# Kernel tuning notes

Measured on AMD Instinct MI355X. Metric: run time of the kernel, lower is better.

The kernel has to match this reference:

```python
import jax, jax.numpy as jnp
import numpy as np

BN_EPS = 1e-5

def batchnorm2d(x, gamma, beta):
    # x: [B, H, *, *]; normalize over (B, dim2, dim3) per channel H (training-mode batch stats)
    mean = jnp.mean(x, axis=(0, 2, 3), keepdims=True)
    var = jnp.var(x, axis=(0, 2, 3), keepdims=True)
    xhat = (x - mean) * jax.lax.rsqrt(var + BN_EPS)
    return xhat * gamma[None, :, None, None] + beta[None, :, None, None]

def setup_inputs() -> dict:
    key = jax.random.key(0)
    ks = jax.random.split(key, 8)
    B, N, C = 64, 196, 768
    H = 12
    hd = C // H  # 64
    patch = 196  # img_size**2, must equal N
    x = jax.random.normal(ks[0], (B, N, C), dtype=jnp.float32)
    W_qv = jax.random.normal(ks[1], (C, 2 * C), dtype=jnp.float32) * (1.0 / np.sqrt(C))
    k_ext = jax.random.normal(ks[2], (patch, hd), dtype=jnp.float32)  # torch init: ones; randomized for testing
    attn_bias = jax.random.normal(ks[3], (1, patch), dtype=jnp.float32) * 0.02
    bn_gamma = jnp.ones((H,), dtype=jnp.float32) + 0.1 * jax.random.normal(ks[4], (H,), dtype=jnp.float32)
    bn_beta = 0.1 * jax.random.normal(ks[5], (H,), dtype=jnp.float32)
    W_proj = jax.random.normal(ks[6], (C, C), dtype=jnp.float32) * (1.0 / np.sqrt(C))
    b_proj = jnp.zeros((C,), dtype=jnp.float32)
    return {"x": x, "W_qv": W_qv, "k_ext": k_ext, "attn_bias": attn_bias,
            "bn_gamma": bn_gamma, "bn_beta": bn_beta, "W_proj": W_proj, "b_proj": b_proj}

def reference(x, W_qv, k_ext, attn_bias, bn_gamma, bn_beta, W_proj, b_proj):
    B, N, C = x.shape
    H = bn_gamma.shape[0]
    hd = C // H
    scale = hd ** -0.5
    # qv projection: [B,N,2C] -> q,v each [B,H,N,hd]
    qv = (x @ W_qv).reshape(B, N, 2, H, hd).transpose(2, 0, 3, 1, 4)
    q, v = qv[0], qv[1]
    # scores against fixed k_ext: [B,H,N,patch]
    attn = jnp.einsum('bhnd,pd->bhnp', q, k_ext)
    attn = (batchnorm2d(attn, bn_gamma, bn_beta) + attn_bias) * scale
    attn = jax.nn.softmax(attn, axis=-1)
    v = batchnorm2d(v, bn_gamma, bn_beta)
    out = jnp.einsum('bhnp,bhpd->bhnd', attn, v)  # patch == N
    out = out.transpose(0, 2, 1, 3).reshape(B, N, C)
    return out @ W_proj + b_proj
```

## Files before the change

### kernel.cpp

```cpp
#include <hip/hip_runtime.h>
#include <hip/hip_bf16.h>

typedef __bf16 b16;
typedef __bf16 b16x4 __attribute__((ext_vector_type(4)));
typedef __bf16 b16x8 __attribute__((ext_vector_type(8)));
typedef float  f32x4 __attribute__((ext_vector_type(4)));

#define B_   64
#define N_   196
#define C_   768
#define H_   12
#define HD_  64
#define TOK  (B_*N_)
#define SCALE 0.125f

__device__ __forceinline__ void gl_lds16(const void* g, void* l){
  __builtin_amdgcn_global_load_lds((const __attribute__((address_space(1))) void*)g,
                                   (__attribute__((address_space(3))) void*)l, 16, 0, 0);
}

__global__ __launch_bounds__(256) void k_transpose_cvt(const float* __restrict__ in,
                                                       b16* __restrict__ out, int R, int C){
  __shared__ b16 tile[32][33];
  int tx = threadIdx.x, ty = threadIdx.y;
  int bx = blockIdx.x, by = blockIdx.y;
  int c = bx*32 + tx;
  #pragma unroll
  for (int i = 0; i < 32; i += 8){
    int r = by*32 + ty + i;
    tile[ty+i][tx] = (b16)in[(long)r*C + c];
  }
  __syncthreads();
  int rr = by*32 + tx;
  #pragma unroll
  for (int i = 0; i < 32; i += 8){
    int cc = bx*32 + ty + i;
    out[(long)cc*R + rr] = tile[tx][ty+i];
  }
}

__global__ __launch_bounds__(256) void k_cvt(const float* __restrict__ in, b16* __restrict__ out){
  long i = ((long)blockIdx.x*256 + threadIdx.x)*8;
  const float4* s = (const float4*)(in + i);
  float4 f0 = s[0], f1 = s[1];
  b16x8 v; v[0]=(b16)f0.x; v[1]=(b16)f0.y; v[2]=(b16)f0.z; v[3]=(b16)f0.w;
           v[4]=(b16)f1.x; v[5]=(b16)f1.y; v[6]=(b16)f1.z; v[7]=(b16)f1.w;
  *(b16x8*)(out + i) = v;
}

__global__ __launch_bounds__(256) void k_kprep(const float* __restrict__ k_ext,
                                               float* __restrict__ Kmat, float* __restrict__ ksum){
  __shared__ float ks[N_][HD_];
  int tid = threadIdx.x, blk = blockIdx.x;
  for (int i = tid; i < N_*HD_; i += 256) ks[i/HD_][i%HD_] = k_ext[i];
  __syncthreads();
  int i = tid >> 2;
  int j0 = blk*16 + (tid & 3)*4;
  float a0=0.f, a1=0.f, a2=0.f, a3=0.f;
  for (int p = 0; p < N_; ++p){
    float ki = ks[p][i];
    float4 kv = *(const float4*)&ks[p][j0];
    a0 += ki*kv.x; a1 += ki*kv.y; a2 += ki*kv.z; a3 += ki*kv.w;
  }
  Kmat[i*64+j0+0]=a0; Kmat[i*64+j0+1]=a1; Kmat[i*64+j0+2]=a2; Kmat[i*64+j0+3]=a3;
  if (blk == 0 && tid < 64){
    float s = 0.f;
    for (int p = 0; p < N_; ++p) s += ks[p][tid];
    ksum[tid] = s;
  }
}

template<int MODE>
__global__ __launch_bounds__(256) void k_gemm(const b16* __restrict__ A,
                                              const b16* __restrict__ BT,
                                              b16* __restrict__ qout, b16* __restrict__ vout,
                                              float* __restrict__ fout, const float* __restrict__ bias,
                                              const float* __restrict__ ksum, float* __restrict__ stats){
  const int NT  = (MODE == 0) ? 12 : 6;
  const int NWG = 98*NT;
  int orig = blockIdx.x;
  int q8 = NWG >> 3, r8 = NWG & 7;
  int xcd = orig & 7, loc = orig >> 3;
  int bid = (xcd < r8 ? xcd*(q8+1) : r8*(q8+1) + (xcd-r8)*q8) + loc;
  int rt = bid / NT, ct = bid % NT;
  int brow = rt*128, bcol = ct*128;

  __shared__ b16 sm[2][2][128*32];
  int tid = threadIdx.x, lane = tid & 63, w = tid >> 6;
  int wr = w >> 1, wc = w & 1;

  int rsub = w*16 + (lane>>2);
  int gsrc = (lane & 3) ^ ((lane >> 3) & 3);
  const b16* gA = A  + (long)(brow + rsub)*768 + gsrc*8;
  const b16* gB = BT + (long)(bcol + rsub)*768 + gsrc*8;
  b16* lA0 = &sm[0][0][w*16*32];
  b16* lB0 = &sm[0][1][w*16*32];
  b16* lA1 = &sm[1][0][w*16*32];
  b16* lB1 = &sm[1][1][w*16*32];

#define STAGE(la, lb, kt) do{ \
    gl_lds16(gA + (kt)*32,            (la));        \
    gl_lds16(gA + (kt)*32 + 64*768,   (la) + 64*32);\
    gl_lds16(gB + (kt)*32,            (lb));        \
    gl_lds16(gB + (kt)*32 + 64*768,   (lb) + 64*32);\
  } while(0)

#define COMPUTE(cur) do{ \
    const char* smA = (const char*)sm[cur][0]; \
    const char* smB = (const char*)sm[cur][1]; \
    b16x8 af[4], bf[4]; \
    _Pragma("unroll") \
    for (int m = 0; m < 4; ++m){ \
      int row = wr*64 + m*16 + (lane & 15); \
      af[m] = *(const b16x8*)(smA + row*64 + (((lane>>4) ^ ((row>>1)&3))<<4)); \
    } \
    _Pragma("unroll") \
    for (int n = 0; n < 4; ++n){ \
      int row = wc*64 + n*16 + (lane & 15); \
      bf[n] = *(const b16x8*)(smB + row*64 + (((lane>>4) ^ ((row>>1)&3))<<4)); \
    } \
    _Pragma("unroll") \
    for (int m = 0; m < 4; ++m) \
      _Pragma("unroll") \
      for (int n = 0; n < 4; ++n) \
        acc[m][n] = __builtin_amdgcn_mfma_f32_16x16x32_bf16(bf[n], af[m], acc[m][n], 0, 0, 0); \
  } while(0)

  f32x4 acc[4][4];
  #pragma unroll
  for (int m = 0; m < 4; ++m)
    #pragma unroll
    for (int n = 0; n < 4; ++n) acc[m][n] = (f32x4){0.f,0.f,0.f,0.f};

  STAGE(lA0, lB0, 0);
  STAGE(lA1, lB1, 1);

  #pragma unroll 1
  for (int kt = 0; kt < 23; ++kt){
    int cur = kt & 1;
    asm volatile("s_waitcnt vmcnt(4)" ::: "memory");
    __builtin_amdgcn_s_barrier();
    asm volatile("" ::: "memory");
    COMPUTE(cur);
    asm volatile("" ::: "memory");
    __builtin_amdgcn_s_barrier();
    asm volatile("" ::: "memory");
    if (kt < 22){
      if (cur == 0) STAGE(lA0, lB0, kt+2);
      else          STAGE(lA1, lB1, kt+2);
    }
  }
  asm volatile("s_waitcnt vmcnt(0)" ::: "memory");
  __builtin_amdgcn_s_barrier();
  asm volatile("" ::: "memory");
  COMPUTE(1);
#undef COMPUTE
#undef STAGE

  if constexpr (MODE == 0){
    bool isV = (bcol >= 768);
    b16* dst = isV ? vout : qout;
    int cb0 = bcol - (isV ? 768 : 0) + wc*64;
    #pragma unroll
    for (int m = 0; m < 4; ++m){
      int r2 = brow + wr*64 + m*16 + (lane & 15);
      #pragma unroll
      for (int n = 0; n < 4; ++n){
        int cc = cb0 + n*16 + ((lane>>4)<<2);
        b16x4 pv;
        #pragma unroll
        for (int j = 0; j < 4; ++j) pv[j] = (b16)acc[m][n][j];
        *(b16x4*)(dst + (long)r2*768 + cc) = pv;
      }
    }
    {
      float a_acc = 0.f, b_acc = 0.f;
      #pragma unroll
      for (int n = 0; n < 4; ++n)
        #pragma unroll
        for (int j = 0; j < 4; ++j){
          int d = n*16 + ((lane>>4)<<2) + j;
          float s = 0.f, s2 = 0.f;
          #pragma unroll
          for (int m = 0; m < 4; ++m){
            float v = acc[m][n][j];
            s += v; s2 += v*v;
          }
          if (isV){ a_acc += s; b_acc += s2; }
          else      a_acc += s * ksum[d];
        }
      #pragma unroll
      for (int off = 1; off < 64; off <<= 1){
        a_acc += __shfl_xor(a_acc, off, 64);
        b_acc += __shfl_xor(b_acc, off, 64);
      }
      if (lane == 0){
        if (isV){
          int hv = 2*(ct - 6) + wc;
          atomicAdd(&stats[24 + hv], a_acc);
          atomicAdd(&stats[36 + hv], b_acc);
        } else {
          int hq = 2*ct + wc;
          atomicAdd(&stats[hq], a_acc);
        }
      }
    }
  } else {
    #pragma unroll
    for (int m = 0; m < 4; ++m){
      int r2 = brow + wr*64 + m*16 + (lane & 15);
      #pragma unroll
      for (int n = 0; n < 4; ++n){
        int cc = bcol + wc*64 + n*16 + ((lane>>4)<<2);
        f32x4 bv = *(const f32x4*)(bias + cc);
        f32x4 o;
        #pragma unroll
        for (int j = 0; j < 4; ++j) o[j] = acc[m][n][j] + bv[j];
        *(f32x4*)(fout + (long)r2*768 + cc) = o;
      }
    }
  }
}

__global__ __launch_bounds__(256) void k_gram(const b16* __restrict__ qb, float* __restrict__ G){
  __shared__ b16 qT[64*232];
  int tid = threadIdx.x, lane = tid & 63, w = tid >> 6;
  int h = blockIdx.x % 12, bg = blockIdx.x / 12;
  f32x4 acc[4];
  #pragma unroll
  for (int n = 0; n < 4; ++n) acc[n] = (f32x4){0.f,0.f,0.f,0.f};
  #pragma unroll 1
  for (int r = 0; r < 2; ++r){
    int b = bg*2 + r;
    const b16* src = qb + (long)(b*196)*768 + h*64;
    int d = lane;
    for (int p0 = w*8; p0 < 224; p0 += 32){
      b16x8 w8;
      #pragma unroll
      for (int j = 0; j < 8; ++j){
        int p = p0 + j;
        w8[j] = (p < 196) ? src[(long)p*768 + d] : (b16)0.f;
      }
      *(b16x8*)(qT + d*232 + p0) = w8;
    }
    __syncthreads();
    #pragma unroll
    for (int ks = 0; ks < 7; ++ks){
      int t0 = ks*32;
      b16x8 af = *(const b16x8*)(qT + (16*w + (lane&15))*232 + t0 + ((lane>>4)<<3));
      #pragma unroll
      for (int n = 0; n < 4; ++n){
        b16x8 bf = *(const b16x8*)(qT + (16*n + (lane&15))*232 + t0 + ((lane>>4)<<3));
        acc[n] = __builtin_amdgcn_mfma_f32_16x16x32_bf16(af, bf, acc[n], 0, 0, 0);
      }
    }
    __syncthreads();
  }
  float* Gh = G + h*4096;
  #pragma unroll
  for (int n = 0; n < 4; ++n)
    #pragma unroll
    for (int j = 0; j < 4; ++j){
      int i  = 16*w + ((lane>>4)<<2) + j;
      int jj = 16*n + (lane&15);
      atomicAdd(&Gh[i*64 + jj], acc[n][j]);
    }
}

__global__ __launch_bounds__(256) void k_sfin(const float* __restrict__ G, const float* __restrict__ Kmat,
                                              const float* __restrict__ stats, const float* __restrict__ gamma,
                                              const float* __restrict__ beta, float* __restrict__ coef){
  int h = blockIdx.x, tid = threadIdx.x;
  const float* Gh = G + h*4096;
  float s = 0.f;
  #pragma unroll
  for (int k = 0; k < 16; ++k) s += Gh[tid + k*256]*Kmat[tid + k*256];
  #pragma unroll
  for (int off = 1; off < 64; off <<= 1) s += __shfl_xor(s, off, 64);
  __shared__ float red[4];
  if ((tid & 63) == 0) red[tid>>6] = s;
  __syncthreads();
  if (tid == 0){
    float S2 = red[0]+red[1]+red[2]+red[3];
    const float cntS = 2458624.f, cntV = 802816.f;
    float S1 = stats[h], VS = stats[24+h], VS2 = stats[36+h];
    float ms = S1/cntS;
    float vars = S2/cntS - ms*ms;
    float alpha = gamma[h]*SCALE*rsqrtf(vars + 1e-5f);
    float mv = VS/cntV;
    float varv = VS2/cntV - mv*mv;
    float a = gamma[h]*rsqrtf(varv + 1e-5f);
    coef[h*4+0] = alpha;
    coef[h*4+1] = a;
    coef[h*4+2] = beta[h] - a*mv;
  }
}

__global__ __launch_bounds__(256, 2) void k_attn(const b16* __restrict__ qb, const b16* __restrict__ vb,
                                                 const float* __restrict__ k_ext,
                                                 const float* __restrict__ attn_bias,
                                                 const float* __restrict__ coef,
                                                 b16* __restrict__ Ob){
  __shared__ b16 ksh[196*64];
  __shared__ b16 vsh[64*216];
  __shared__ b16 psh[4][16*200];
  __shared__ float bsh[196];

  int tid = threadIdx.x, lane = tid & 63, wid = tid >> 6;
  int bh = blockIdx.x;
  int h = bh % 12, b = bh / 12;
  const b16* qt = qb + (long)(b*196)*768 + h*64;
  const b16* vt = vb + (long)(b*196)*768 + h*64;
  float alpha = coef[h*4+0], av = coef[h*4+1], cv = coef[h*4+2];

  for (int c = tid; c < 196*8; c += 256){
    int p = c >> 3, g = c & 7;
    const float4* src = (const float4*)(k_ext + p*64 + g*8);
    float4 f0 = src[0], f1 = src[1];
    b16x8 v; v[0]=(b16)f0.x; v[1]=(b16)f0.y; v[2]=(b16)f0.z; v[3]=(b16)f0.w;
             v[4]=(b16)f1.x; v[5]=(b16)f1.y; v[6]=(b16)f1.z; v[7]=(b16)f1.w;
    *(b16x8*)((char*)ksh + p*128 + ((g ^ (p&7))<<4)) = v;
  }
  for (int p = tid; p < 196; p += 256) bsh[p] = attn_bias[p]*SCALE;
  {
    int d = tid & 63;
    for (int p0 = (tid>>6)*8; p0 < 196; p0 += 32){
      b16x8 w;
      #pragma unroll
      for (int j = 0; j < 8; ++j){
        int p = p0 + j;
        w[j] = (p < 196) ? vt[(long)p*768 + d] : (b16)0.f;
      }
      *(b16x8*)((char*)vsh + d*432 + p0*2) = w;
    }
  }
  __syncthreads();

  for (int rt = wid; rt < 13; rt += 4){
    int n0 = rt*16;
    int qrow = n0 + (lane & 15); if (qrow > 195) qrow = 195;
    b16x8 a0 = *(const b16x8*)((const char*)qt + (long)qrow*1536 +      ((lane>>4)<<4));
    b16x8 a1 = *(const b16x8*)((const char*)qt + (long)qrow*1536 + 64 + ((lane>>4)<<4));

    f32x4 sc[13];
    #pragma unroll
    for (int ct = 0; ct < 13; ++ct){
      int p = ct*16 + (lane & 15); int pc = p > 195 ? 195 : p;
      b16x8 b0 = *(const b16x8*)((const char*)ksh + pc*128 + ((( (lane>>4))   ^ (pc&7))<<4));
      b16x8 b1 = *(const b16x8*)((const char*)ksh + pc*128 + (((4+(lane>>4))  ^ (pc&7))<<4));
      f32x4 z = {0.f,0.f,0.f,0.f};
      z = __builtin_amdgcn_mfma_f32_16x16x32_bf16(a0, b0, z, 0, 0, 0);
      z = __builtin_amdgcn_mfma_f32_16x16x32_bf16(a1, b1, z, 0, 0, 0);
      sc[ct] = z;
    }
    int pcol = lane & 15;
    float mx[4] = {-1e30f,-1e30f,-1e30f,-1e30f};
    #pragma unroll
    for (int ct = 0; ct < 13; ++ct){
      int p = ct*16 + pcol;
      bool valid = (p < 196);
      float badd = valid ? bsh[p < 196 ? p : 0] : 0.f;
      #pragma unroll
      for (int j = 0; j < 4; ++j){
        float lv = valid ? (sc[ct][j]*alpha + badd) : -1e30f;
        sc[ct][j] = lv;
        mx[j] = fmaxf(mx[j], lv);
      }
    }
    #pragma unroll
    for (int off = 1; off < 16; off <<= 1)
      #pragma unroll
      for (int j = 0; j < 4; ++j) mx[j] = fmaxf(mx[j], __shfl_xor(mx[j], off, 64));
    float sm[4] = {0.f,0.f,0.f,0.f};
    #pragma unroll
    for (int ct = 0; ct < 13; ++ct)
      #pragma unroll
      for (int j = 0; j < 4; ++j){
        float e = __expf(sc[ct][j] - mx[j]);
        sc[ct][j] = e; sm[j] += e;
      }
    #pragma unroll
    for (int off = 1; off < 16; off <<= 1)
      #pragma unroll
      for (int j = 0; j < 4; ++j) sm[j] += __shfl_xor(sm[j], off, 64);
    float rs[4];
    #pragma unroll
    for (int j = 0; j < 4; ++j) rs[j] = 1.f/sm[j];

    b16* pw = psh[wid];
    #pragma unroll
    for (int ct = 0; ct < 12; ++ct){
      int p = ct*16 + pcol;
      #pragma unroll
      for (int j = 0; j < 4; ++j){
        int r = ((lane>>4)<<2) + j;
        pw[r*200 + p] = (b16)(sc[ct][j]*rs[j]);
      }
    }
    float pt12[4];
    #pragma unroll
    for (int j = 0; j < 4; ++j) pt12[j] = sc[12][j]*rs[j];

    __asm__ volatile("s_waitcnt lgkmcnt(0)" ::: "memory");
    __builtin_amdgcn_sched_barrier(0);

    f32x4 o[4];
    #pragma unroll
    for (int dt = 0; dt < 4; ++dt) o[dt] = (f32x4){0.f,0.f,0.f,0.f};
    #pragma unroll
    for (int pt = 0; pt < 6; ++pt){
      b16x8 pa = *(const b16x8*)((const char*)pw + (lane&15)*400 + pt*64 + ((lane>>4)<<4));
      #pragma unroll
      for (int dt = 0; dt < 4; ++dt){
        b16x8 vf = *(const b16x8*)((const char*)vsh + (dt*16 + (lane&15))*432 + pt*64 + ((lane>>4)<<4));
        o[dt] = __builtin_amdgcn_mfma_f32_16x16x32_bf16(pa, vf, o[dt], 0, 0, 0);
      }
    }
    #pragma unroll
    for (int e = 0; e < 4; ++e){
      float pe[4];
      #pragma unroll
      for (int j = 0; j < 4; ++j) pe[j] = __shfl(pt12[j], (lane & 48) + e, 64);
      #pragma unroll
      for (int dt = 0; dt < 4; ++dt){
        b16 vv = *((const b16*)((const char*)vsh + (dt*16 + (lane&15))*432 + (192+e)*2));
        float vvf = (float)vv;
        #pragma unroll
        for (int j = 0; j < 4; ++j) o[dt][j] += pe[j]*vvf;
      }
    }
    #pragma unroll
    for (int dt = 0; dt < 4; ++dt)
      #pragma unroll
      for (int j = 0; j < 4; ++j){
        int n = n0 + ((lane>>4)<<2) + j;
        if (n < 196){
          long idx = ((long)(b*196 + n))*768 + h*64 + dt*16 + (lane&15);
          Ob[idx] = (b16)(av*o[dt][j] + cv);
        }
      }
  }
}

extern "C" void kernel_launch(void* const* d_in, const int* in_sizes, int n_in,
                              void* d_out, int out_size, void* d_ws, size_t ws_size,
                              hipStream_t stream){
  const float* x         = (const float*)d_in[0];
  const float* W_qv      = (const float*)d_in[1];
  const float* k_ext     = (const float*)d_in[2];
  const float* attn_bias = (const float*)d_in[3];
  const float* bn_gamma  = (const float*)d_in[4];
  const float* bn_beta   = (const float*)d_in[5];
  const float* W_proj    = (const float*)d_in[6];
  const float* b_proj    = (const float*)d_in[7];
  float* out = (float*)d_out;

  char* ws = (char*)d_ws;
  const long SZ = 19267584;
  b16*   q_buf   = (b16*)(ws);
  b16*   v_buf   = (b16*)(ws + SZ);
  b16*   O_buf   = (b16*)(ws + 2*SZ);
  b16*   x_bf16  = (b16*)(ws + 2*SZ);
  b16*   W_qvT   = (b16*)(ws + 3*SZ);
  b16*   W_projT = (b16*)(ws + 3*SZ + 2359296);
  float* Kmat    = (float*)(ws + 3*SZ + 3538944);
  float* ksum    = Kmat + 4096;
  float* stats   = ksum + 64;
  float* coef    = stats + 48;
  float* Ggram   = coef + 48;

  hipMemsetAsync(stats, 0, 48*sizeof(float), stream);
  hipMemsetAsync(Ggram, 0, 12*4096*sizeof(float), stream);

  dim3 tb(32, 8);
  k_transpose_cvt<<<dim3(1536/32, 768/32), tb, 0, stream>>>(W_qv,   W_qvT,   768, 1536);
  k_transpose_cvt<<<dim3(768/32,  768/32), tb, 0, stream>>>(W_proj, W_projT, 768, 768);
  k_cvt<<<4704, 256, 0, stream>>>(x, x_bf16);
  k_kprep<<<4, 256, 0, stream>>>(k_ext, Kmat, ksum);
  k_gemm<0><<<98*12, 256, 0, stream>>>(x_bf16, W_qvT, q_buf, v_buf, nullptr, nullptr, ksum, stats);
  k_gram<<<384, 256, 0, stream>>>(q_buf, Ggram);
  k_sfin<<<12, 256, 0, stream>>>(Ggram, Kmat, stats, bn_gamma, bn_beta, coef);
  k_attn<<<768, 256, 0, stream>>>(q_buf, v_buf, k_ext, attn_bias, coef, O_buf);
  k_gemm<1><<<98*6, 256, 0, stream>>>(O_buf, W_projT, nullptr, nullptr, out, b_proj, nullptr, nullptr);
}
```

Measured before the change: 196.6 us.

## Replace LDS double-buffered GEMM staging with direct global-to-register MFMA operand loads

The GEMM kernel drops the shared-memory double buffer fed by global_load_lds, along with its barriers. Each wave now loads its MFMA A and B fragments straight from global memory into registers, with the k-loop unrolled by four. This removes LDS traffic and workgroup synchronisation. In exchange the two waves that share a row or column tile each fetch it separately, and loads lose the coalesced, swizzled staging, so more pressure falls on the L2 cache and global bandwidth.

Result: slower. 288.0 us (+46.5%).

```diff
diff --git a/kernel.cpp b/kernel.cpp
--- a/kernel.cpp
+++ b/kernel.cpp
@@ -13,11 +13,6 @@
 #define HD_  64
 #define TOK  (B_*N_)
 #define SCALE 0.125f
-
-__device__ __forceinline__ void gl_lds16(const void* g, void* l){
-  __builtin_amdgcn_global_load_lds((const __attribute__((address_space(1))) void*)g,
-                                   (__attribute__((address_space(3))) void*)l, 16, 0, 0);
-}
 
 __global__ __launch_bounds__(256) void k_transpose_cvt(const float* __restrict__ in,
                                                        b16* __restrict__ out, int R, int C){
@@ -83,48 +78,14 @@
   int xcd = orig & 7, loc = orig >> 3;
   int bid = (xcd < r8 ? xcd*(q8+1) : r8*(q8+1) + (xcd-r8)*q8) + loc;
   int rt = bid / NT, ct = bid % NT;
-  int brow = rt*128, bcol = ct*128;
-
-  __shared__ b16 sm[2][2][128*32];
+
   int tid = threadIdx.x, lane = tid & 63, w = tid >> 6;
   int wr = w >> 1, wc = w & 1;
-
-  int rsub = w*16 + (lane>>2);
-  int gsrc = (lane & 3) ^ ((lane >> 3) & 3);
-  const b16* gA = A  + (long)(brow + rsub)*768 + gsrc*8;
-  const b16* gB = BT + (long)(bcol + rsub)*768 + gsrc*8;
-  b16* lA0 = &sm[0][0][w*16*32];
-  b16* lB0 = &sm[0][1][w*16*32];
-  b16* lA1 = &sm[1][0][w*16*32];
-  b16* lB1 = &sm[1][1][w*16*32];
-
-#define STAGE(la, lb, kt) do{ \
-    gl_lds16(gA + (kt)*32,            (la));        \
-    gl_lds16(gA + (kt)*32 + 64*768,   (la) + 64*32);\
-    gl_lds16(gB + (kt)*32,            (lb));        \
-    gl_lds16(gB + (kt)*32 + 64*768,   (lb) + 64*32);\
-  } while(0)
-
-#define COMPUTE(cur) do{ \
-    const char* smA = (const char*)sm[cur][0]; \
-    const char* smB = (const char*)sm[cur][1]; \
-    b16x8 af[4], bf[4]; \
-    _Pragma("unroll") \
-    for (int m = 0; m < 4; ++m){ \
-      int row = wr*64 + m*16 + (lane & 15); \
-      af[m] = *(const b16x8*)(smA + row*64 + (((lane>>4) ^ ((row>>1)&3))<<4)); \
-    } \
-    _Pragma("unroll") \
-    for (int n = 0; n < 4; ++n){ \
-      int row = wc*64 + n*16 + (lane & 15); \
-      bf[n] = *(const b16x8*)(smB + row*64 + (((lane>>4) ^ ((row>>1)&3))<<4)); \
-    } \
-    _Pragma("unroll") \
-    for (int m = 0; m < 4; ++m) \
-      _Pragma("unroll") \
-      for (int n = 0; n < 4; ++n) \
-        acc[m][n] = __builtin_amdgcn_mfma_f32_16x16x32_bf16(bf[n], af[m], acc[m][n], 0, 0, 0); \
-  } while(0)
+  int brow = rt*128 + wr*64;
+  int bcol = ct*128 + wc*64;
+
+  const b16* pa = A  + (long)(brow + (lane & 15))*768 + ((lane >> 4) << 3);
+  const b16* pb = BT + (long)(bcol + (lane & 15))*768 + ((lane >> 4) << 3);
 
   f32x4 acc[4][4];
   #pragma unroll
@@ -132,38 +93,27 @@
     #pragma unroll
     for (int n = 0; n < 4; ++n) acc[m][n] = (f32x4){0.f,0.f,0.f,0.f};
 
-  STAGE(lA0, lB0, 0);
-  STAGE(lA1, lB1, 1);
-
-  #pragma unroll 1
-  for (int kt = 0; kt < 23; ++kt){
-    int cur = kt & 1;
-    asm volatile("s_waitcnt vmcnt(4)" ::: "memory");
-    __builtin_amdgcn_s_barrier();
-    asm volatile("" ::: "memory");
-    COMPUTE(cur);
-    asm volatile("" ::: "memory");
-    __builtin_amdgcn_s_barrier();
-    asm volatile("" ::: "memory");
-    if (kt < 22){
-      if (cur == 0) STAGE(lA0, lB0, kt+2);
-      else          STAGE(lA1, lB1, kt+2);
-    }
-  }
-  asm volatile("s_waitcnt vmcnt(0)" ::: "memory");
-  __builtin_amdgcn_s_barrier();
-  asm volatile("" ::: "memory");
-  COMPUTE(1);
-#undef COMPUTE
-#undef STAGE
+  #pragma unroll 4
+  for (int kt = 0; kt < 24; ++kt){
+    b16x8 af[4], bf[4];
+    #pragma unroll
+    for (int m = 0; m < 4; ++m) af[m] = *(const b16x8*)(pa + (long)m*16*768 + kt*32);
+    #pragma unroll
+    for (int n = 0; n < 4; ++n) bf[n] = *(const b16x8*)(pb + (long)n*16*768 + kt*32);
+    #pragma unroll
+    for (int m = 0; m < 4; ++m)
+      #pragma unroll
+      for (int n = 0; n < 4; ++n)
+        acc[m][n] = __builtin_amdgcn_mfma_f32_16x16x32_bf16(bf[n], af[m], acc[m][n], 0, 0, 0);
+  }
 
   if constexpr (MODE == 0){
     bool isV = (bcol >= 768);
     b16* dst = isV ? vout : qout;
-    int cb0 = bcol - (isV ? 768 : 0) + wc*64;
+    int cb0 = bcol - (isV ? 768 : 0);
     #pragma unroll
     for (int m = 0; m < 4; ++m){
-      int r2 = brow + wr*64 + m*16 + (lane & 15);
+      int r2 = brow + m*16 + (lane & 15);
       #pragma unroll
       for (int n = 0; n < 4; ++n){
         int cc = cb0 + n*16 + ((lane>>4)<<2);
@@ -208,10 +158,10 @@
   } else {
     #pragma unroll
     for (int m = 0; m < 4; ++m){
-      int r2 = brow + wr*64 + m*16 + (lane & 15);
+      int r2 = brow + m*16 + (lane & 15);
       #pragma unroll
       for (int n = 0; n < 4; ++n){
-        int cc = bcol + wc*64 + n*16 + ((lane>>4)<<2);
+        int cc = bcol + n*16 + ((lane>>4)<<2);
         f32x4 bv = *(const f32x4*)(bias + cc);
         f32x4 o;
         #pragma unroll
```

## Enlarge GEMM tiles to 256x256 with 512-thread workgroups

Applied to the files above, without the earlier changes.

Both bf16 GEMMs (qv projection and output projection) now use 256x256 output tiles computed by 8 waves in a 2x4 layout, each wave holding an 8x4 grid of 16x16 MFMA accumulators. The goal is better operand reuse from LDS and less global traffic per FLOP. The trade-off is far fewer workgroups (294 and 147) on a 256-CU part, which leaves CUs idle or unevenly loaded. It also raises register pressure through 128 accumulator floats per lane and adds an lgkmcnt wait before the barrier.

Measured after the change: 194.6 us. Within noise of the previous version (-1.0%).

```diff
diff --git a/kernel.cpp b/kernel.cpp
--- a/kernel.cpp
+++ b/kernel.cpp
@@ -71,69 +71,65 @@
 }
 
 template<int MODE>
-__global__ __launch_bounds__(256) void k_gemm(const b16* __restrict__ A,
-                                              const b16* __restrict__ BT,
-                                              b16* __restrict__ qout, b16* __restrict__ vout,
-                                              float* __restrict__ fout, const float* __restrict__ bias,
-                                              const float* __restrict__ ksum, float* __restrict__ stats){
-  const int NT  = (MODE == 0) ? 12 : 6;
-  const int NWG = 98*NT;
+__global__ __launch_bounds__(512, 2) void k_gemm(const b16* __restrict__ A,
+                                                 const b16* __restrict__ BT,
+                                                 b16* __restrict__ qout, b16* __restrict__ vout,
+                                                 float* __restrict__ fout, const float* __restrict__ bias,
+                                                 const float* __restrict__ ksum, float* __restrict__ stats){
+  const int NT  = (MODE == 0) ? 6 : 3;
+  const int NWG = 49*NT;
   int orig = blockIdx.x;
   int q8 = NWG >> 3, r8 = NWG & 7;
   int xcd = orig & 7, loc = orig >> 3;
   int bid = (xcd < r8 ? xcd*(q8+1) : r8*(q8+1) + (xcd-r8)*q8) + loc;
   int rt = bid / NT, ct = bid % NT;
-  int brow = rt*128, bcol = ct*128;
-
-  __shared__ b16 sm[2][2][128*32];
+  int brow = rt*256, bcol = ct*256;
+
+  __shared__ char smc[2*32768];
   int tid = threadIdx.x, lane = tid & 63, w = tid >> 6;
-  int wr = w >> 1, wc = w & 1;
-
-  int rsub = w*16 + (lane>>2);
+  int wr = w >> 2, wc = w & 3;
+
   int gsrc = (lane & 3) ^ ((lane >> 3) & 3);
-  const b16* gA = A  + (long)(brow + rsub)*768 + gsrc*8;
-  const b16* gB = BT + (long)(bcol + rsub)*768 + gsrc*8;
-  b16* lA0 = &sm[0][0][w*16*32];
-  b16* lB0 = &sm[0][1][w*16*32];
-  b16* lA1 = &sm[1][0][w*16*32];
-  b16* lB1 = &sm[1][1][w*16*32];
-
-#define STAGE(la, lb, kt) do{ \
-    gl_lds16(gA + (kt)*32,            (la));        \
-    gl_lds16(gA + (kt)*32 + 64*768,   (la) + 64*32);\
-    gl_lds16(gB + (kt)*32,            (lb));        \
-    gl_lds16(gB + (kt)*32 + 64*768,   (lb) + 64*32);\
+  const b16* gA = A  + (long)(brow + w*16 + (lane>>2))*768 + gsrc*8;
+  const b16* gB = BT + (long)(bcol + w*16 + (lane>>2))*768 + gsrc*8;
+
+#define STAGE(cur, t) do{ \
+    char* ba = smc + (cur)*32768; \
+    gl_lds16(gA + (long)(t)*32,           ba + (w*16)*64); \
+    gl_lds16(gA + (long)(t)*32 + 128*768, ba + (128 + w*16)*64); \
+    gl_lds16(gB + (long)(t)*32,           ba + 16384 + (w*16)*64); \
+    gl_lds16(gB + (long)(t)*32 + 128*768, ba + 16384 + (128 + w*16)*64); \
   } while(0)
 
 #define COMPUTE(cur) do{ \
-    const char* smA = (const char*)sm[cur][0]; \
-    const char* smB = (const char*)sm[cur][1]; \
-    b16x8 af[4], bf[4]; \
+    const char* ba = smc + (cur)*32768; \
+    const char* bb = ba + 16384; \
+    b16x8 af[8], bf[4]; \
     _Pragma("unroll") \
-    for (int m = 0; m < 4; ++m){ \
-      int row = wr*64 + m*16 + (lane & 15); \
-      af[m] = *(const b16x8*)(smA + row*64 + (((lane>>4) ^ ((row>>1)&3))<<4)); \
+    for (int m = 0; m < 8; ++m){ \
+      int row = wr*128 + m*16 + (lane & 15); \
+      af[m] = *(const b16x8*)(ba + row*64 + (((lane>>4) ^ ((row>>1)&3))<<4)); \
     } \
     _Pragma("unroll") \
     for (int n = 0; n < 4; ++n){ \
       int row = wc*64 + n*16 + (lane & 15); \
-      bf[n] = *(const b16x8*)(smB + row*64 + (((lane>>4) ^ ((row>>1)&3))<<4)); \
+      bf[n] = *(const b16x8*)(bb + row*64 + (((lane>>4) ^ ((row>>1)&3))<<4)); \
     } \
     _Pragma("unroll") \
-    for (int m = 0; m < 4; ++m) \
+    for (int m = 0; m < 8; ++m) \
       _Pragma("unroll") \
       for (int n = 0; n < 4; ++n) \
         acc[m][n] = __builtin_amdgcn_mfma_f32_16x16x32_bf16(bf[n], af[m], acc[m][n], 0, 0, 0); \
   } while(0)
 
-  f32x4 acc[4][4];
-  #pragma unroll
-  for (int m = 0; m < 4; ++m)
+  f32x4 acc[8][4];
+  #pragma unroll
+  for (int m = 0; m < 8; ++m)
     #pragma unroll
     for (int n = 0; n < 4; ++n) acc[m][n] = (f32x4){0.f,0.f,0.f,0.f};
 
-  STAGE(lA0, lB0, 0);
-  STAGE(lA1, lB1, 1);
+  STAGE(0, 0);
+  STAGE(1, 1);
 
   #pragma unroll 1
   for (int kt = 0; kt < 23; ++kt){
@@ -142,13 +138,10 @@
     __builtin_amdgcn_s_barrier();
     asm volatile("" ::: "memory");
     COMPUTE(cur);
-    asm volatile("" ::: "memory");
+    asm volatile("s_waitcnt lgkmcnt(0)" ::: "memory");
     __builtin_amdgcn_s_barrier();
     asm volatile("" ::: "memory");
-    if (kt < 22){
-      if (cur == 0) STAGE(lA0, lB0, kt+2);
-      else          STAGE(lA1, lB1, kt+2);
-    }
+    if (kt < 22) STAGE(cur, kt+2);
   }
   asm volatile("s_waitcnt vmcnt(0)" ::: "memory");
   __builtin_amdgcn_s_barrier();
@@ -158,12 +151,13 @@
 #undef STAGE
 
   if constexpr (MODE == 0){
-    bool isV = (bcol >= 768);
+    int hidx = ct*4 + wc;
+    bool isV = (hidx >= 12);
     b16* dst = isV ? vout : qout;
-    int cb0 = bcol - (isV ? 768 : 0) + wc*64;
-    #pragma unroll
-    for (int m = 0; m < 4; ++m){
-      int r2 = brow + wr*64 + m*16 + (lane & 15);
+    int cb0 = bcol + wc*64 - (isV ? 768 : 0);
+    #pragma unroll
+    for (int m = 0; m < 8; ++m){
+      int r2 = brow + wr*128 + m*16 + (lane & 15);
       #pragma unroll
       for (int n = 0; n < 4; ++n){
         int cc = cb0 + n*16 + ((lane>>4)<<2);
@@ -182,7 +176,7 @@
           int d = n*16 + ((lane>>4)<<2) + j;
           float s = 0.f, s2 = 0.f;
           #pragma unroll
-          for (int m = 0; m < 4; ++m){
+          for (int m = 0; m < 8; ++m){
             float v = acc[m][n][j];
             s += v; s2 += v*v;
           }
@@ -196,19 +190,17 @@
       }
       if (lane == 0){
         if (isV){
-          int hv = 2*(ct - 6) + wc;
-          atomicAdd(&stats[24 + hv], a_acc);
-          atomicAdd(&stats[36 + hv], b_acc);
+          atomicAdd(&stats[24 + (hidx-12)], a_acc);
+          atomicAdd(&stats[36 + (hidx-12)], b_acc);
         } else {
-          int hq = 2*ct + wc;
-          atomicAdd(&stats[hq], a_acc);
+          atomicAdd(&stats[hidx], a_acc);
         }
       }
     }
   } else {
     #pragma unroll
-    for (int m = 0; m < 4; ++m){
-      int r2 = brow + wr*64 + m*16 + (lane & 15);
+    for (int m = 0; m < 8; ++m){
+      int r2 = brow + wr*128 + m*16 + (lane & 15);
       #pragma unroll
       for (int n = 0; n < 4; ++n){
         int cc = bcol + wc*64 + n*16 + ((lane>>4)<<2);
@@ -477,9 +469,9 @@
   k_transpose_cvt<<<dim3(768/32,  768/32), tb, 0, stream>>>(W_proj, W_projT, 768, 768);
   k_cvt<<<4704, 256, 0, stream>>>(x, x_bf16);
   k_kprep<<<4, 256, 0, stream>>>(k_ext, Kmat, ksum);
-  k_gemm<0><<<98*12, 256, 0, stream>>>(x_bf16, W_qvT, q_buf, v_buf, nullptr, nullptr, ksum, stats);
+  k_gemm<0><<<49*6, 512, 0, stream>>>(x_bf16, W_qvT, q_buf, v_buf, nullptr, nullptr, ksum, stats);
   k_gram<<<384, 256, 0, stream>>>(q_buf, Ggram);
   k_sfin<<<12, 256, 0, stream>>>(Ggram, Kmat, stats, bn_gamma, bn_beta, coef);
   k_attn<<<768, 256, 0, stream>>>(q_buf, v_buf, k_ext, attn_bias, coef, O_buf);
-  k_gemm<1><<<98*6, 256, 0, stream>>>(O_buf, W_projT, nullptr, nullptr, out, b_proj, nullptr, nullptr);
-}
+  k_gemm<1><<<49*3, 512, 0, stream>>>(O_buf, W_projT, nullptr, nullptr, out, b_proj, nullptr, nullptr);
+}
```
